# Kernel tuning notes

Measured on AMD Instinct MI355X. Metric: run time of the kernel, lower is better.

The kernel has to match this reference:

```python
import jax, jax.numpy as jnp
import numpy as np

D = 384      # d_model
H = 6        # num_heads
K = 8        # k_neighbors
B = 8        # batch
N = 2048     # num points
EPS = 1e-5


def _layer_norm(x, g, b):
    m = jnp.mean(x, axis=-1, keepdims=True)
    v = jnp.var(x, axis=-1, keepdims=True)
    return (x - m) * jax.lax.rsqrt(v + EPS) * g + b


def setup_inputs() -> dict:
    key = jax.random.key(0)
    ks = jax.random.split(key, 12)
    s = 0.02
    return {
        "coords": jax.random.normal(ks[0], (B, 3, N), jnp.float32),
        "features": jax.random.normal(ks[1], (B, D, N), jnp.float32),
        "ln1_g": jnp.ones((D,), jnp.float32),
        "ln1_b": jnp.zeros((D,), jnp.float32),
        "w_qkv": jax.random.normal(ks[2], (D, 3 * D), jnp.float32) * s,
        "w_attn_out": jax.random.normal(ks[3], (D, D), jnp.float32) * s,
        "b_attn_out": jnp.zeros((D,), jnp.float32),
        "ga_wq": jax.random.normal(ks[4], (D, D), jnp.float32) * s,
        "ga_wk": jax.random.normal(ks[5], (D, D), jnp.float32) * s,
        "ga_wv": jax.random.normal(ks[6], (D, D), jnp.float32) * s,
        "merge_w": jax.random.normal(ks[7], (2 * D, D), jnp.float32) * s,
        "merge_b": jnp.zeros((D,), jnp.float32),
        "ln2_g": jnp.ones((D,), jnp.float32),
        "ln2_b": jnp.zeros((D,), jnp.float32),
        "ff_w1": jax.random.normal(ks[8], (D, 2 * D), jnp.float32) * s,
        "ff_b1": jnp.zeros((2 * D,), jnp.float32),
        "ff_w2": jax.random.normal(ks[9], (2 * D, D), jnp.float32) * s,
        "ff_b2": jnp.zeros((D,), jnp.float32),
    }


def reference(coords, features, ln1_g, ln1_b, w_qkv, w_attn_out, b_attn_out,
              ga_wq, ga_wk, ga_wv, merge_w, merge_b, ln2_g, ln2_b,
              ff_w1, ff_b1, ff_w2, ff_b2):
    b, d, n = features.shape
    dh = d // H
    f = jnp.swapaxes(features, 1, 2)          # [B, N, D]
    nf = _layer_norm(f, ln1_g, ln1_b)         # [B, N, D]

    # --- dense multi-head self-attention branch ---
    qkv = nf @ w_qkv                           # [B, N, 3D]
    q, k, v = jnp.split(qkv, 3, axis=-1)
    def heads(x):
        return x.reshape(b, n, H, dh).transpose(0, 2, 1, 3)  # [B, H, N, dh]
    scores = jnp.einsum('bhqd,bhkd->bhqk', heads(q), heads(k)) / jnp.sqrt(jnp.float32(dh))
    attn = jnp.einsum('bhqk,bhkd->bhqd', jax.nn.softmax(scores, axis=-1), heads(v))
    attn = attn.transpose(0, 2, 1, 3).reshape(b, n, d)
    attn = attn @ w_attn_out + b_attn_out      # output projection

    # --- KNN graph-attention branch over normalized features ---
    c = jnp.swapaxes(coords, 1, 2)             # [B, N, 3]
    sq = jnp.sum(c * c, axis=-1)               # [B, N]
    d2 = sq[:, :, None] + sq[:, None, :] - 2.0 * jnp.einsum('bnd,bmd->bnm', c, c)
    _, idx = jax.lax.top_k(-d2, K)             # [B, N, K] nearest-neighbor indices
    nbrs = jax.vmap(lambda fe, i: fe[i])(nf, idx)  # [B, N, K, D]
    gq = nf @ ga_wq                             # [B, N, D]
    gk = nbrs @ ga_wk                           # [B, N, K, D]
    gv = nbrs @ ga_wv
    gs = jnp.einsum('bnd,bnkd->bnk', gq, gk) / jnp.sqrt(jnp.float32(d))
    geom = jnp.einsum('bnk,bnkd->bnd', jax.nn.softmax(gs, axis=-1), gv)  # [B, N, D]

    # --- merge + residual + FFN ---
    merged = jnp.concatenate([attn, geom], axis=-1) @ merge_w + merge_b
    f = f + merged
    h = _layer_norm(f, ln2_g, ln2_b)
    f = f + (jax.nn.gelu(h @ ff_w1 + ff_b1) @ ff_w2 + ff_b2)
    return jnp.swapaxes(f, 1, 2)               # [B, D, N]
```

## Files before the change

### kernel.cpp

```cpp
#include <hip/hip_runtime.h>
#include <hip/hip_bf16.h>
#include <cstdint>

#define D_MODEL 384
#define NHEAD 6
#define DHEAD 64
#define NPTS 2048
#define BATCH 8

typedef __attribute__((ext_vector_type(8))) short short8;
typedef __attribute__((ext_vector_type(4))) float floatx4;
typedef __attribute__((ext_vector_type(2))) unsigned int u32x2;
typedef __attribute__((ext_vector_type(4))) unsigned int u32x4;

__device__ __forceinline__ float bf2f(unsigned short u) {
    return __uint_as_float(((unsigned int)u) << 16);
}

__device__ __forceinline__ unsigned short f2bf(float f) {
    unsigned int u = __float_as_uint(f);
    unsigned int r = (u + 0x7FFFu + ((u >> 16) & 1u)) >> 16;
    return (unsigned short)r;
}

__device__ __forceinline__ unsigned cvtpk(float lo, float hi) {
    unsigned r;
    asm("v_cvt_pk_bf16_f32 %0, %1, %2" : "=v"(r) : "v"(lo), "v"(hi));
    return r;
}

#define TR16(dst, addr, imm) \
    asm volatile("ds_read_b64_tr_b16 %0, %1 offset:" #imm : "=v"(dst) : "v"(addr))

__device__ __forceinline__ float gelu_tanh(float x) {
    float x3 = x * x * x;
    return 0.5f * x * (1.0f + tanhf(0.7978845608028654f * (x + 0.044715f * x3)));
}

__device__ __forceinline__ void gload_lds16(const unsigned short* g, unsigned short* l) {
    __builtin_amdgcn_global_load_lds(
        (const __attribute__((address_space(1))) unsigned int*)g,
        (__attribute__((address_space(3))) unsigned int*)l, 16, 0, 0);
}

__global__ __launch_bounds__(256) void k_wprep(
    const float* __restrict__ wqkv, const float* __restrict__ wao,
    const float* __restrict__ wq, const float* __restrict__ wk,
    const float* __restrict__ wv, const float* __restrict__ wm,
    const float* __restrict__ w1, const float* __restrict__ w2,
    unsigned short* __restrict__ qkvT, unsigned short* __restrict__ aoT,
    unsigned short* __restrict__ gaT, unsigned short* __restrict__ mT,
    unsigned short* __restrict__ f1T, unsigned short* __restrict__ f2T) {
    __shared__ float tile[32][33];
    int id = blockIdx.x;
    const float* src;
    unsigned short* dst;
    int K, N;
    if (id < 432)       {            src = wqkv; dst = qkvT;            K = 384; N = 1152; }
    else if (id < 576)  { id -= 432; src = wao;  dst = aoT;             K = 384; N = 384; }
    else if (id < 720)  { id -= 576; src = wq;   dst = gaT;             K = 384; N = 384; }
    else if (id < 864)  { id -= 720; src = wk;   dst = gaT + 384 * 384; K = 384; N = 384; }
    else if (id < 1008) { id -= 864; src = wv;   dst = gaT + 768 * 384; K = 384; N = 384; }
    else if (id < 1296) { id -= 1008; src = wm;  dst = mT;              K = 768; N = 384; }
    else if (id < 1584) { id -= 1296; src = w1;  dst = f1T;             K = 384; N = 768; }
    else                { id -= 1584; src = w2;  dst = f2T;             K = 768; N = 384; }
    int ntiles = N >> 5;
    int nt = id % ntiles, kt = id / ntiles;
    int tx = threadIdx.x, ty = threadIdx.y;
#pragma unroll
    for (int i = 0; i < 32; i += 8)
        tile[ty + i][tx] = src[(size_t)(kt * 32 + ty + i) * N + nt * 32 + tx];
    __syncthreads();
#pragma unroll
    for (int i = 0; i < 32; i += 8)
        dst[(size_t)(nt * 32 + ty + i) * K + kt * 32 + tx] = f2bf(tile[tx][ty + i]);
}

__global__ __launch_bounds__(256) void k_transpose_in(const float* __restrict__ feat,
                                                      unsigned short* __restrict__ f) {
    __shared__ float tile[32][33];
    int b = blockIdx.z;
    int n0 = blockIdx.x * 32, d0 = blockIdx.y * 32;
    int tx = threadIdx.x, ty = threadIdx.y;
#pragma unroll
    for (int i = 0; i < 32; i += 8)
        tile[ty + i][tx] = feat[((size_t)b * D_MODEL + d0 + ty + i) * NPTS + n0 + tx];
    __syncthreads();
#pragma unroll
    for (int i = 0; i < 32; i += 8)
        f[((size_t)b * NPTS + n0 + ty + i) * D_MODEL + d0 + tx] = f2bf(tile[tx][ty + i]);
}

__global__ __launch_bounds__(256) void k_transpose_out(const unsigned short* __restrict__ f,
                                                       float* __restrict__ out) {
    __shared__ float tile[32][33];
    int b = blockIdx.z;
    int d0 = blockIdx.x * 32, n0 = blockIdx.y * 32;
    int tx = threadIdx.x, ty = threadIdx.y;
#pragma unroll
    for (int i = 0; i < 32; i += 8)
        tile[ty + i][tx] = bf2f(f[((size_t)b * NPTS + n0 + ty + i) * D_MODEL + d0 + tx]);
    __syncthreads();
#pragma unroll
    for (int i = 0; i < 32; i += 8)
        out[((size_t)b * D_MODEL + d0 + ty + i) * NPTS + n0 + tx] = tile[tx][ty + i];
}

__global__ __launch_bounds__(256) void k_vt(const unsigned short* __restrict__ qkv,
                                            unsigned short* __restrict__ vt) {
    __shared__ unsigned short tile[32][33];
    int b = blockIdx.z;
    int h = blockIdx.y >> 1, d0 = (blockIdx.y & 1) * 32;
    int n0 = blockIdx.x * 32;
    int tx = threadIdx.x, ty = threadIdx.y;
#pragma unroll
    for (int i = 0; i < 32; i += 8)
        tile[ty + i][tx] =
            qkv[((size_t)b * NPTS + n0 + ty + i) * 1152 + 768 + h * 64 + d0 + tx];
    __syncthreads();
#pragma unroll
    for (int i = 0; i < 32; i += 8)
        vt[(((size_t)(b * NHEAD + h) * 64) + d0 + ty + i) * NPTS + n0 + tx] = tile[tx][ty + i];
}

__global__ __launch_bounds__(128) void k_layernorm(const unsigned short* __restrict__ x,
                                                   const float* __restrict__ g,
                                                   const float* __restrict__ bt,
                                                   unsigned short* __restrict__ y) {
    int row = blockIdx.x, t = threadIdx.x;
    const unsigned short* xr = x + (size_t)row * D_MODEL;
    float v0 = bf2f(xr[t]), v1 = bf2f(xr[t + 128]), v2 = bf2f(xr[t + 256]);
    float s = v0 + v1 + v2;
    float s2 = v0 * v0 + v1 * v1 + v2 * v2;
#pragma unroll
    for (int off = 32; off > 0; off >>= 1) {
        s += __shfl_xor(s, off, 64);
        s2 += __shfl_xor(s2, off, 64);
    }
    __shared__ float ps[2], ps2[2];
    if ((t & 63) == 0) { ps[t >> 6] = s; ps2[t >> 6] = s2; }
    __syncthreads();
    s = ps[0] + ps[1];
    s2 = ps2[0] + ps2[1];
    float mean = s * (1.0f / 384.0f);
    float var = s2 * (1.0f / 384.0f) - mean * mean;
    var = fmaxf(var, 0.0f);
    float inv = 1.0f / sqrtf(var + 1e-5f);
    unsigned short* yr = y + (size_t)row * D_MODEL;
    yr[t]       = f2bf((v0 - mean) * inv * g[t]       + bt[t]);
    yr[t + 128] = f2bf((v1 - mean) * inv * g[t + 128] + bt[t + 128]);
    yr[t + 256] = f2bf((v2 - mean) * inv * g[t + 256] + bt[t + 256]);
}

__global__ __launch_bounds__(256) void k_knn(const float* __restrict__ coords,
                                             int* __restrict__ idx) {
    __shared__ float4 cpts[NPTS];
    int b = blockIdx.x >> 9;
    int q0 = (blockIdx.x & 511) * 4;
    const float* cb = coords + (size_t)b * 3 * NPTS;
    int tid = threadIdx.x;
#pragma unroll
    for (int i = 0; i < 8; i++) {
        int m = tid + i * 256;
        float x = cb[m], y = cb[NPTS + m], z = cb[2 * NPTS + m];
        float sq = __fadd_rn(__fadd_rn(__fmul_rn(x, x), __fmul_rn(y, y)), __fmul_rn(z, z));
        cpts[m] = make_float4(x, y, z, sq);
    }
    __syncthreads();
    int wv = tid >> 6, lane = tid & 63;
    int n = q0 + wv;
    float4 qp = cpts[n];
    float qx = qp.x, qy = qp.y, qz = qp.z, sqn = qp.w;
    unsigned keys[32];
    unsigned h[8];
#pragma unroll
    for (int k = 0; k < 8; k++) h[k] = 0xFFFFFFFFu;
#pragma unroll
    for (int j = 0; j < 32; j++) {
        float4 cp = cpts[j * 64 + lane];
        float dot = __fadd_rn(__fadd_rn(__fmul_rn(qx, cp.x), __fmul_rn(qy, cp.y)),
                              __fmul_rn(qz, cp.z));
        float d2 = __fsub_rn(__fadd_rn(sqn, cp.w), __fmul_rn(2.0f, dot));
        unsigned u = __float_as_uint(d2);
        u ^= (unsigned)(((int)u >> 31)) | 0x80000000u;
        keys[j] = u;
        unsigned cur = u;
#pragma unroll
        for (int t2 = 0; t2 < 8; t2++) {
            unsigned lo = h[t2] < cur ? h[t2] : cur;
            cur = h[t2] < cur ? cur : h[t2];
            h[t2] = lo;
        }
    }
    unsigned curh = h[0];
    unsigned T8 = 0;
#pragma unroll
    for (int r = 0; r < 8; r++) {
        unsigned w = curh;
#pragma unroll
        for (int off = 1; off < 64; off <<= 1) {
            unsigned o = __shfl_xor(w, off, 64);
            w = o < w ? o : w;
        }
        T8 = w;
        if (r < 7) {
            unsigned long long mask = __ballot(curh == w);
            if (curh == w && (mask & ((1ull << lane) - 1ull)) == 0) {
#pragma unroll
                for (int t2 = 0; t2 < 7; t2++) h[t2] = h[t2 + 1];
                h[7] = 0xFFFFFFFFu;
                curh = h[0];
            }
        }
    }
    int* outr = idx + ((size_t)b * NPTS + n) * 8;
    int cnt = 0;
    unsigned meq = 0xFFFFFFFFu;
#pragma unroll
    for (int j = 0; j < 32; j++) {
        unsigned m = (unsigned)(j * 64 + lane);
        bool strict = keys[j] < T8;
        unsigned long long msk = __ballot(strict);
        if (strict) {
            int pos = cnt + (int)__popcll(msk & ((1ull << lane) - 1ull));
            outr[pos] = (int)m;
        }
        cnt += (int)__popcll(msk);
        if (keys[j] == T8 && m < meq) meq = m;
    }
    while (cnt < 8) {
        unsigned w = meq;
#pragma unroll
        for (int off = 1; off < 64; off <<= 1) {
            unsigned o = __shfl_xor(w, off, 64);
            w = o < w ? o : w;
        }
        bool winner = (meq == w);
        if (winner) outr[cnt] = (int)w;
        cnt++;
        if (cnt >= 8) break;
        if (winner) {
            meq = 0xFFFFFFFFu;
#pragma unroll
            for (int j = 0; j < 32; j++) {
                unsigned m = (unsigned)(j * 64 + lane);
                if (keys[j] == T8 && m > w && m < meq) meq = m;
            }
        }
    }
}

__global__ __launch_bounds__(256) void k_gemm(const unsigned short* __restrict__ A, int lda,
                                              const unsigned short* __restrict__ WT,
                                              const float* __restrict__ bias,
                                              const unsigned short* __restrict__ res,
                                              unsigned short* __restrict__ C, int ldc,
                                              int K, int act) {
    __shared__ unsigned short Alds[2 * 128 * 32];
    __shared__ unsigned short Wlds[2 * 128 * 32];
    int tid = threadIdx.x;
    int wv = tid >> 6, lane = tid & 63;
    int l15 = lane & 15, quad = lane >> 4;
    int row0 = blockIdx.y * 128, col0 = blockIdx.x * 128;
    int wm = wv >> 1, wn = wv & 1;
    int wbase = tid & 192;
    floatx4 acc[4][4];
#pragma unroll
    for (int i = 0; i < 4; i++)
#pragma unroll
        for (int j = 0; j < 4; j++) acc[i][j] = (floatx4){0.f, 0.f, 0.f, 0.f};
    for (int k0 = 0; k0 < K; k0 += 64) {
#pragma unroll
        for (int i = 0; i < 4; i++) {
            int idx = i * 256 + tid;
            int kc = idx >> 9, row = (idx >> 2) & 127, ko = idx & 3;
            unsigned short* ldst = Alds + (size_t)(i * 256 + wbase) * 8;
            gload_lds16(A + (size_t)(row0 + row) * lda + k0 + kc * 32 + ko * 8, ldst);
            unsigned short* ldstw = Wlds + (size_t)(i * 256 + wbase) * 8;
            gload_lds16(WT + (size_t)(col0 + row) * K + k0 + kc * 32 + ko * 8, ldstw);
        }
        __syncthreads();
#pragma unroll
        for (int kc = 0; kc < 2; kc++) {
            short8 af[4], bf[4];
#pragma unroll
            for (int i = 0; i < 4; i++)
                af[i] = *(const short8*)&Alds[kc * 4096 + (wm * 64 + i * 16 + l15) * 32 + quad * 8];
#pragma unroll
            for (int j = 0; j < 4; j++)
                bf[j] = *(const short8*)&Wlds[kc * 4096 + (wn * 64 + j * 16 + l15) * 32 + quad * 8];
#pragma unroll
            for (int i = 0; i < 4; i++)
#pragma unroll
                for (int j = 0; j < 4; j++)
                    acc[i][j] =
                        __builtin_amdgcn_mfma_f32_16x16x32_bf16(bf[j], af[i], acc[i][j], 0, 0, 0);
        }
        __syncthreads();
    }
#pragma unroll
    for (int i = 0; i < 4; i++) {
        int r = row0 + wm * 64 + i * 16 + l15;
#pragma unroll
        for (int j = 0; j < 4; j++) {
            int cb = col0 + wn * 64 + j * 16 + quad * 4;
            float4 bv = bias ? *(const float4*)(bias + cb) : make_float4(0.f, 0.f, 0.f, 0.f);
            float v0 = acc[i][j][0] + bv.x;
            float v1 = acc[i][j][1] + bv.y;
            float v2 = acc[i][j][2] + bv.z;
            float v3 = acc[i][j][3] + bv.w;
            if (act == 1) {
                v0 = gelu_tanh(v0); v1 = gelu_tanh(v1);
                v2 = gelu_tanh(v2); v3 = gelu_tanh(v3);
            }
            if (res) {
                uint2 rv = *(const uint2*)(res + (size_t)r * ldc + cb);
                const unsigned short* rs = (const unsigned short*)&rv;
                v0 += bf2f(rs[0]); v1 += bf2f(rs[1]);
                v2 += bf2f(rs[2]); v3 += bf2f(rs[3]);
            }
            ushort4 u;
            u.x = f2bf(v0); u.y = f2bf(v1); u.z = f2bf(v2); u.w = f2bf(v3);
            *(ushort4*)(C + (size_t)r * ldc + cb) = u;
        }
    }
}

__global__ __launch_bounds__(256, 3) void k_attn(const unsigned short* __restrict__ qkv,
                                                 const unsigned short* __restrict__ vt,
                                                 unsigned short* __restrict__ attn) {
    __shared__ unsigned short Klds[2][64 * 64];
    __shared__ unsigned short VTl[2][64 * 64];
    __shared__ unsigned short Pt[4][2048];
    int b = blockIdx.z, h = blockIdx.y;
    int tid = threadIdx.x;
    int wv = tid >> 6, lane = tid & 63;
    int l15 = lane & 15, quad = lane >> 4;
    int qbase = blockIdx.x * 128 + wv * 32;
    const unsigned short* qkvb = qkv + (size_t)b * NPTS * 1152;
    const unsigned short* vtb = vt + (size_t)(b * NHEAD + h) * 64 * NPTS;
    const float SC = 0.18033688011112042f;
    short8 qf[2][2];
#pragma unroll
    for (int qt = 0; qt < 2; qt++) {
        const unsigned short* qptr =
            qkvb + (size_t)(qbase + qt * 16 + l15) * 1152 + h * 64 + quad * 8;
        qf[qt][0] = *(const short8*)qptr;
        qf[qt][1] = *(const short8*)(qptr + 32);
#pragma unroll
        for (int g = 0; g < 2; g++) {
            short8 v = qf[qt][g];
#pragma unroll
            for (int e = 0; e < 8; e++)
                v[e] = (short)f2bf(bf2f((unsigned short)v[e]) * SC);
            qf[qt][g] = v;
        }
    }
    short8 ones;
#pragma unroll
    for (int e = 0; e < 8; e++) ones[e] = (short)0x3F80;
    int x7 = l15 & 7;
    int sk0 = ((quad ^ x7) << 4);
    int sk1 = (((quad + 4) ^ x7) << 4);
    unsigned pa = (unsigned)(size_t)(__attribute__((address_space(3))) unsigned short*)&Pt[wv][0] +
                  (unsigned)(quad * 256 + l15 * 2);
    int sdg = tid & 7;
    floatx4 o[2][4];
#pragma unroll
    for (int qt = 0; qt < 2; qt++)
#pragma unroll
        for (int ct = 0; ct < 4; ct++) o[qt][ct] = (floatx4){0.f, 0.f, 0.f, 0.f};
    floatx4 l4[2];
    l4[0] = (floatx4){0.f, 0.f, 0.f, 0.f};
    l4[1] = (floatx4){0.f, 0.f, 0.f, 0.f};

    auto stage = [&](int c, int k0) {
#pragma unroll
        for (int i = 0; i < 2; i++) {
            int id = i * 256 + tid;
            int row = id >> 3;
            int sl = sdg ^ (row & 7);
            gload_lds16(qkvb + (size_t)(k0 + row) * 1152 + 384 + h * 64 + sl * 8,
                        &Klds[c][(size_t)(i * 256 + (tid & 192)) * 8]);
            gload_lds16(vtb + (size_t)row * NPTS + k0 + sl * 8,
                        &VTl[c][(size_t)(i * 256 + (tid & 192)) * 8]);
        }
    };

    stage(0, 0);
    __syncthreads();
    for (int t = 0; t < 32; ++t) {
        int c = t & 1;
        if (t < 31) stage(c ^ 1, (t + 1) * 64);
        const char* Kb = (const char*)&Klds[c][0];
        const char* Vb = (const char*)&VTl[c][0];
        short8 kf[4][2];
#pragma unroll
        for (int ct = 0; ct < 4; ct++) {
            kf[ct][0] = *(const short8*)(Kb + (ct * 16 + l15) * 128 + sk0);
            kf[ct][1] = *(const short8*)(Kb + (ct * 16 + l15) * 128 + sk1);
        }
#pragma unroll
        for (int qt = 0; qt < 2; qt++) {
            floatx4 s4[4];
#pragma unroll
            for (int ct = 0; ct < 4; ct++) {
                floatx4 z = (floatx4){0.f, 0.f, 0.f, 0.f};
                z = __builtin_amdgcn_mfma_f32_16x16x32_bf16(qf[qt][0], kf[ct][0], z, 0, 0, 0);
                z = __builtin_amdgcn_mfma_f32_16x16x32_bf16(qf[qt][1], kf[ct][1], z, 0, 0, 0);
                s4[ct] = z;
            }
#pragma unroll
            for (int ct = 0; ct < 4; ct++) {
                float p0 = __builtin_amdgcn_exp2f(s4[ct][0]);
                float p1 = __builtin_amdgcn_exp2f(s4[ct][1]);
                float p2 = __builtin_amdgcn_exp2f(s4[ct][2]);
                float p3 = __builtin_amdgcn_exp2f(s4[ct][3]);
                u32x2 pk;
                pk.x = cvtpk(p0, p1);
                pk.y = cvtpk(p2, p3);
                *(u32x2*)&Pt[wv][qt * 1024 + (ct * 16 + l15) * 16 + quad * 4] = pk;
            }
        }
        short8 vf[4][2];
#pragma unroll
        for (int ct = 0; ct < 4; ct++) {
            vf[ct][0] = *(const short8*)(Vb + (ct * 16 + l15) * 128 + sk0);
            vf[ct][1] = *(const short8*)(Vb + (ct * 16 + l15) * 128 + sk1);
        }
        asm volatile("s_waitcnt lgkmcnt(0)" ::: "memory");
        u32x2 q0g0l, q0g0h, q0g1l, q0g1h, q1g0l, q1g0h, q1g1l, q1g1h;
        TR16(q0g0l, pa, 0);
        TR16(q0g0h, pa, 128);
        TR16(q0g1l, pa, 1024);
        TR16(q0g1h, pa, 1152);
        TR16(q1g0l, pa, 2048);
        TR16(q1g0h, pa, 2176);
        TR16(q1g1l, pa, 3072);
        TR16(q1g1h, pa, 3200);
        asm volatile("s_waitcnt lgkmcnt(0)" ::: "memory");
        __builtin_amdgcn_sched_barrier(0);
        short8 pf[2][2];
        pf[0][0] = __builtin_bit_cast(short8, (u32x4){q0g0l.x, q0g0l.y, q0g0h.x, q0g0h.y});
        pf[0][1] = __builtin_bit_cast(short8, (u32x4){q0g1l.x, q0g1l.y, q0g1h.x, q0g1h.y});
        pf[1][0] = __builtin_bit_cast(short8, (u32x4){q1g0l.x, q1g0l.y, q1g0h.x, q1g0h.y});
        pf[1][1] = __builtin_bit_cast(short8, (u32x4){q1g1l.x, q1g1l.y, q1g1h.x, q1g1h.y});
#pragma unroll
        for (int ct = 0; ct < 4; ct++) {
#pragma unroll
            for (int qt = 0; qt < 2; qt++) {
                o[qt][ct] = __builtin_amdgcn_mfma_f32_16x16x32_bf16(vf[ct][0], pf[qt][0], o[qt][ct], 0, 0, 0);
                o[qt][ct] = __builtin_amdgcn_mfma_f32_16x16x32_bf16(vf[ct][1], pf[qt][1], o[qt][ct], 0, 0, 0);
            }
        }
#pragma unroll
        for (int qt = 0; qt < 2; qt++) {
            l4[qt] = __builtin_amdgcn_mfma_f32_16x16x32_bf16(ones, pf[qt][0], l4[qt], 0, 0, 0);
            l4[qt] = __builtin_amdgcn_mfma_f32_16x16x32_bf16(ones, pf[qt][1], l4[qt], 0, 0, 0);
        }
        if (t < 31) __syncthreads();
    }
#pragma unroll
    for (int qt = 0; qt < 2; qt++) {
        float linv = 1.0f / l4[qt][0];
#pragma unroll
        for (int ct = 0; ct < 4; ct++) {
            ushort4 u;
            u.x = f2bf(o[qt][ct][0] * linv);
            u.y = f2bf(o[qt][ct][1] * linv);
            u.z = f2bf(o[qt][ct][2] * linv);
            u.w = f2bf(o[qt][ct][3] * linv);
            *(ushort4*)(attn + ((size_t)b * NPTS + qbase + qt * 16 + l15) * 384 + h * 64 +
                        ct * 16 + quad * 4) = u;
        }
    }
}

__global__ __launch_bounds__(64) void k_geom(const unsigned short* __restrict__ gap,
                                             const int* __restrict__ idx,
                                             unsigned short* __restrict__ cat) {
    int r = blockIdx.x;
    int b = r >> 11;
    int t = threadIdx.x;
    int nb[8];
#pragma unroll
    for (int k = 0; k < 8; k++) nb[k] = idx[(size_t)r * 8 + k];
    const unsigned short* gqr = gap + (size_t)r * 1152;
    float qv[6];
#pragma unroll
    for (int j = 0; j < 6; j++) qv[j] = bf2f(gqr[t + 64 * j]);
    float s[8];
#pragma unroll
    for (int k = 0; k < 8; k++) {
        const unsigned short* nkr = gap + ((size_t)b * NPTS + nb[k]) * 1152 + 384;
        float acc = 0.0f;
#pragma unroll
        for (int j = 0; j < 6; j++) acc += qv[j] * bf2f(nkr[t + 64 * j]);
#pragma unroll
        for (int mm = 32; mm > 0; mm >>= 1) acc += __shfl_xor(acc, mm, 64);
        s[k] = acc * 0.05103103630798287f;
    }
    float mx = s[0];
#pragma unroll
    for (int k = 1; k < 8; k++) mx = fmaxf(mx, s[k]);
    float w[8];
    float sum = 0.0f;
#pragma unroll
    for (int k = 0; k < 8; k++) { w[k] = __expf(s[k] - mx); sum += w[k]; }
    float inv = 1.0f / sum;
    unsigned short* outr = cat + (size_t)r * 768 + 384;
#pragma unroll
    for (int j = 0; j < 6; j++) {
        int d = t + 64 * j;
        float acc = 0.0f;
#pragma unroll
        for (int k = 0; k < 8; k++)
            acc += w[k] * bf2f(gap[((size_t)b * NPTS + nb[k]) * 1152 + 768 + d]);
        outr[d] = f2bf(acc * inv);
    }
}

extern "C" void kernel_launch(void* const* d_in, const int* in_sizes, int n_in,
                              void* d_out, int out_size, void* d_ws, size_t ws_size,
                              hipStream_t stream) {
    (void)in_sizes; (void)n_in; (void)out_size; (void)ws_size;
    const float* coords     = (const float*)d_in[0];
    const float* features   = (const float*)d_in[1];
    const float* ln1_g      = (const float*)d_in[2];
    const float* ln1_b      = (const float*)d_in[3];
    const float* w_qkv      = (const float*)d_in[4];
    const float* w_attn_out = (const float*)d_in[5];
    const float* b_attn_out = (const float*)d_in[6];
    const float* ga_wq      = (const float*)d_in[7];
    const float* ga_wk      = (const float*)d_in[8];
    const float* ga_wv      = (const float*)d_in[9];
    const float* merge_w    = (const float*)d_in[10];
    const float* merge_b    = (const float*)d_in[11];
    const float* ln2_g      = (const float*)d_in[12];
    const float* ln2_b      = (const float*)d_in[13];
    const float* ff_w1      = (const float*)d_in[14];
    const float* ff_b1      = (const float*)d_in[15];
    const float* ff_w2      = (const float*)d_in[16];
    const float* ff_b2      = (const float*)d_in[17];

    unsigned short* W0 = (unsigned short*)d_ws;
    const size_t SZ = (size_t)BATCH * NPTS * D_MODEL;
    unsigned short* F    = W0 + 0 * SZ;
    unsigned short* NF   = W0 + 1 * SZ;
    unsigned short* QKV  = W0 + 2 * SZ;
    unsigned short* ATTN = W0 + 5 * SZ;
    unsigned short* VT   = W0 + 6 * SZ;
    unsigned short* CAT  = W0 + 2 * SZ;
    unsigned short* GAP  = W0 + 4 * SZ;
    unsigned short* F2   = W0 + 4 * SZ;
    unsigned short* HB   = W0 + 1 * SZ;
    unsigned short* T1   = W0 + 5 * SZ;
    unsigned short* FFIN = W0 + 2 * SZ;
    int*            IDX  = (int*)(W0 + 7 * SZ);
    unsigned short* WTS  = W0 + 7 * SZ + 262144;
    unsigned short* qkvT = WTS;
    unsigned short* aoT  = qkvT + 442368;
    unsigned short* gaT  = aoT + 147456;
    unsigned short* mT   = gaT + 442368;
    unsigned short* f1T  = mT + 294912;
    unsigned short* f2T  = f1T + 294912;

    const int M = BATCH * NPTS;

    k_wprep<<<1872, dim3(32, 8), 0, stream>>>(w_qkv, w_attn_out, ga_wq, ga_wk, ga_wv,
                                              merge_w, ff_w1, ff_w2,
                                              qkvT, aoT, gaT, mT, f1T, f2T);
    k_transpose_in<<<dim3(NPTS / 32, D_MODEL / 32, BATCH), dim3(32, 8), 0, stream>>>(features, F);
    k_layernorm<<<M, 128, 0, stream>>>(F, ln1_g, ln1_b, NF);
    k_knn<<<BATCH * (NPTS / 4), 256, 0, stream>>>(coords, IDX);
    k_gemm<<<dim3(9, M / 128), 256, 0, stream>>>(NF, 384, qkvT, nullptr, nullptr,
                                                 QKV, 1152, 384, 0);
    k_vt<<<dim3(NPTS / 32, 2 * NHEAD, BATCH), dim3(32, 8), 0, stream>>>(QKV, VT);
    k_attn<<<dim3(NPTS / 128, NHEAD, BATCH), 256, 0, stream>>>(QKV, VT, ATTN);
    k_gemm<<<dim3(3, M / 128), 256, 0, stream>>>(ATTN, 384, aoT, b_attn_out, nullptr,
                                                 CAT, 768, 384, 0);
    k_gemm<<<dim3(9, M / 128), 256, 0, stream>>>(NF, 384, gaT, nullptr, nullptr,
                                                 GAP, 1152, 384, 0);
    k_geom<<<M, 64, 0, stream>>>(GAP, IDX, CAT);
    k_gemm<<<dim3(3, M / 128), 256, 0, stream>>>(CAT, 768, mT, merge_b, F,
                                                 F2, 384, 768, 0);
    k_layernorm<<<M, 128, 0, stream>>>(F2, ln2_g, ln2_b, HB);
    k_gemm<<<dim3(6, M / 128), 256, 0, stream>>>(HB, 384, f1T, ff_b1, nullptr,
                                                 T1, 768, 384, 1);
    k_gemm<<<dim3(3, M / 128), 256, 0, stream>>>(T1, 768, f2T, ff_b2, F2,
                                                 FFIN, 384, 768, 0);
    k_transpose_out<<<dim3(D_MODEL / 32, NPTS / 32, BATCH), dim3(32, 8), 0, stream>>>(
        FFIN, (float*)d_out);
}
```

Before: 447.5 us.

## Keep attention probabilities in registers using transposed QK and 16x16x16 MFMA

Computes the score tile as K·Q so the MFMA output layout lines up with the B operand of a 16x16x16 bf16 MFMA. The exponentiated probabilities then feed the PV product directly from registers, which removes the per-wave LDS staging buffer, the transpose reads and the lgkm waits. The trade-off is twice as many smaller MFMAs for PV and for the row-sum, plus narrower 8-byte V reads from LDS.

```diff
diff --git a/kernel.cpp b/kernel.cpp
--- a/kernel.cpp
+++ b/kernel.cpp
@@ -9,9 +9,9 @@
 #define BATCH 8
 
 typedef __attribute__((ext_vector_type(8))) short short8;
+typedef __attribute__((ext_vector_type(4))) short short4v;
 typedef __attribute__((ext_vector_type(4))) float floatx4;
 typedef __attribute__((ext_vector_type(2))) unsigned int u32x2;
-typedef __attribute__((ext_vector_type(4))) unsigned int u32x4;
 
 __device__ __forceinline__ float bf2f(unsigned short u) {
     return __uint_as_float(((unsigned int)u) << 16);
@@ -29,8 +29,15 @@
     return r;
 }
 
-#define TR16(dst, addr, imm) \
-    asm volatile("ds_read_b64_tr_b16 %0, %1 offset:" #imm : "=v"(dst) : "v"(addr))
+__device__ __forceinline__ floatx4 mfma16(short4v a, short4v b, floatx4 c) {
+#if __has_builtin(__builtin_amdgcn_mfma_f32_16x16x16bf16_1k)
+    return __builtin_amdgcn_mfma_f32_16x16x16bf16_1k(a, b, c, 0, 0, 0);
+#else
+    floatx4 d;
+    asm("v_mfma_f32_16x16x16_bf16 %0, %1, %2, %3" : "=v"(d) : "v"(a), "v"(b), "v"(c));
+    return d;
+#endif
+}
 
 __device__ __forceinline__ float gelu_tanh(float x) {
     float x3 = x * x * x;
@@ -331,7 +338,6 @@
                                                  unsigned short* __restrict__ attn) {
     __shared__ unsigned short Klds[2][64 * 64];
     __shared__ unsigned short VTl[2][64 * 64];
-    __shared__ unsigned short Pt[4][2048];
     int b = blockIdx.z, h = blockIdx.y;
     int tid = threadIdx.x;
     int wv = tid >> 6, lane = tid & 63;
@@ -356,14 +362,16 @@
             qf[qt][g] = v;
         }
     }
-    short8 ones;
-#pragma unroll
-    for (int e = 0; e < 8; e++) ones[e] = (short)0x3F80;
+    short4v ones4;
+#pragma unroll
+    for (int e = 0; e < 4; e++) ones4[e] = (short)0x3F80;
     int x7 = l15 & 7;
     int sk0 = ((quad ^ x7) << 4);
     int sk1 = (((quad + 4) ^ x7) << 4);
-    unsigned pa = (unsigned)(size_t)(__attribute__((address_space(3))) unsigned short*)&Pt[wv][0] +
-                  (unsigned)(quad * 256 + l15 * 2);
+    int vslot[4];
+#pragma unroll
+    for (int kt = 0; kt < 4; kt++) vslot[kt] = (((kt * 2 + (quad >> 1)) ^ x7) << 4);
+    int vsub = (quad & 1) * 8;
     int sdg = tid & 7;
     floatx4 o[2][4];
 #pragma unroll
@@ -400,64 +408,42 @@
             kf[ct][0] = *(const short8*)(Kb + (ct * 16 + l15) * 128 + sk0);
             kf[ct][1] = *(const short8*)(Kb + (ct * 16 + l15) * 128 + sk1);
         }
+        short4v pf16[2][4];
 #pragma unroll
         for (int qt = 0; qt < 2; qt++) {
-            floatx4 s4[4];
 #pragma unroll
             for (int ct = 0; ct < 4; ct++) {
                 floatx4 z = (floatx4){0.f, 0.f, 0.f, 0.f};
-                z = __builtin_amdgcn_mfma_f32_16x16x32_bf16(qf[qt][0], kf[ct][0], z, 0, 0, 0);
-                z = __builtin_amdgcn_mfma_f32_16x16x32_bf16(qf[qt][1], kf[ct][1], z, 0, 0, 0);
-                s4[ct] = z;
-            }
-#pragma unroll
-            for (int ct = 0; ct < 4; ct++) {
-                float p0 = __builtin_amdgcn_exp2f(s4[ct][0]);
-                float p1 = __builtin_amdgcn_exp2f(s4[ct][1]);
-                float p2 = __builtin_amdgcn_exp2f(s4[ct][2]);
-                float p3 = __builtin_amdgcn_exp2f(s4[ct][3]);
+                z = __builtin_amdgcn_mfma_f32_16x16x32_bf16(kf[ct][0], qf[qt][0], z, 0, 0, 0);
+                z = __builtin_amdgcn_mfma_f32_16x16x32_bf16(kf[ct][1], qf[qt][1], z, 0, 0, 0);
+                float p0 = __builtin_amdgcn_exp2f(z[0]);
+                float p1 = __builtin_amdgcn_exp2f(z[1]);
+                float p2 = __builtin_amdgcn_exp2f(z[2]);
+                float p3 = __builtin_amdgcn_exp2f(z[3]);
                 u32x2 pk;
                 pk.x = cvtpk(p0, p1);
                 pk.y = cvtpk(p2, p3);
-                *(u32x2*)&Pt[wv][qt * 1024 + (ct * 16 + l15) * 16 + quad * 4] = pk;
+                pf16[qt][ct] = __builtin_bit_cast(short4v, pk);
             }
         }
-        short8 vf[4][2];
-#pragma unroll
-        for (int ct = 0; ct < 4; ct++) {
-            vf[ct][0] = *(const short8*)(Vb + (ct * 16 + l15) * 128 + sk0);
-            vf[ct][1] = *(const short8*)(Vb + (ct * 16 + l15) * 128 + sk1);
-        }
-        asm volatile("s_waitcnt lgkmcnt(0)" ::: "memory");
-        u32x2 q0g0l, q0g0h, q0g1l, q0g1h, q1g0l, q1g0h, q1g1l, q1g1h;
-        TR16(q0g0l, pa, 0);
-        TR16(q0g0h, pa, 128);
-        TR16(q0g1l, pa, 1024);
-        TR16(q0g1h, pa, 1152);
-        TR16(q1g0l, pa, 2048);
-        TR16(q1g0h, pa, 2176);
-        TR16(q1g1l, pa, 3072);
-        TR16(q1g1h, pa, 3200);
-        asm volatile("s_waitcnt lgkmcnt(0)" ::: "memory");
-        __builtin_amdgcn_sched_barrier(0);
-        short8 pf[2][2];
-        pf[0][0] = __builtin_bit_cast(short8, (u32x4){q0g0l.x, q0g0l.y, q0g0h.x, q0g0h.y});
-        pf[0][1] = __builtin_bit_cast(short8, (u32x4){q0g1l.x, q0g1l.y, q0g1h.x, q0g1h.y});
-        pf[1][0] = __builtin_bit_cast(short8, (u32x4){q1g0l.x, q1g0l.y, q1g0h.x, q1g0h.y});
-        pf[1][1] = __builtin_bit_cast(short8, (u32x4){q1g1l.x, q1g1l.y, q1g1h.x, q1g1h.y});
-#pragma unroll
-        for (int ct = 0; ct < 4; ct++) {
-#pragma unroll
-            for (int qt = 0; qt < 2; qt++) {
-                o[qt][ct] = __builtin_amdgcn_mfma_f32_16x16x32_bf16(vf[ct][0], pf[qt][0], o[qt][ct], 0, 0, 0);
-                o[qt][ct] = __builtin_amdgcn_mfma_f32_16x16x32_bf16(vf[ct][1], pf[qt][1], o[qt][ct], 0, 0, 0);
+        const char* vb0 = Vb + l15 * 128 + vsub;
+#pragma unroll
+        for (int ctd = 0; ctd < 4; ctd++) {
+            short4v va[4];
+#pragma unroll
+            for (int kt = 0; kt < 4; kt++)
+                va[kt] = *(const short4v*)(vb0 + ctd * 2048 + vslot[kt]);
+#pragma unroll
+            for (int kt = 0; kt < 4; kt++) {
+#pragma unroll
+                for (int qt = 0; qt < 2; qt++)
+                    o[qt][ctd] = mfma16(va[kt], pf16[qt][kt], o[qt][ctd]);
             }
         }
 #pragma unroll
-        for (int qt = 0; qt < 2; qt++) {
-            l4[qt] = __builtin_amdgcn_mfma_f32_16x16x32_bf16(ones, pf[qt][0], l4[qt], 0, 0, 0);
-            l4[qt] = __builtin_amdgcn_mfma_f32_16x16x32_bf16(ones, pf[qt][1], l4[qt], 0, 0, 0);
-        }
+        for (int qt = 0; qt < 2; qt++)
+#pragma unroll
+            for (int kt = 0; kt < 4; kt++) l4[qt] = mfma16(ones4, pf16[qt][kt], l4[qt]);
         if (t < 31) __syncthreads();
     }
 #pragma unroll
```

New measurement: 437.7 us. 2.2% less time.
